# Kernel tuning notes

Hardware: AMD Instinct MI355X
Metric: run time of the kernel (lower is better)

## Reference

```python
import math
import jax, jax.numpy as jnp
import numpy as np

B, N, C = 2, 2048, 4096
NUM_HEADS, KV_HEADS, HEAD_DIM = 32, 8, 128
N_REP = NUM_HEADS // KV_HEADS  # num_key_value_groups
MAX_SEQ = 4096


def rotate_half(x):
    h = x.shape[-1] // 2
    return jnp.concatenate([-x[..., h:], x[..., :h]], axis=-1)


def setup_inputs() -> dict:
    key = jax.random.key(0)
    k1, k2 = jax.random.split(key)
    inp = jax.random.normal(k1, (B, N, C), jnp.float32)
    sz = NUM_HEADS * HEAD_DIM + 2 * KV_HEADS * HEAD_DIM  # 6144
    weight = jax.random.normal(k2, (sz, C), jnp.float32) * 0.02
    # real LLaMA rotary caches [1,1,MAX_SEQ,HEAD_DIM]
    inv_freq = 1.0 / (10000.0 ** (jnp.arange(0, HEAD_DIM, 2, dtype=jnp.float32) / HEAD_DIM))
    t = jnp.arange(MAX_SEQ, dtype=jnp.float32)
    freqs = jnp.outer(t, inv_freq)
    emb = jnp.concatenate([freqs, freqs], axis=-1)
    cos_cached = jnp.cos(emb)[None, None]
    sin_cached = jnp.sin(emb)[None, None]
    neg = jnp.finfo(jnp.float32).min
    causal = jnp.where(jnp.tril(jnp.ones((N, N), dtype=bool)), 0.0, neg)
    attention_mask = jnp.broadcast_to(causal[None, None], (B, 1, N, N))
    position_ids = jnp.broadcast_to(jnp.arange(N, dtype=jnp.int32), (B, N))
    observation_mask = jnp.ones((B, N), dtype=jnp.int32)
    return dict(input=inp, weight=weight, cos_cached=cos_cached, sin_cached=sin_cached,
                attention_mask=attention_mask, position_ids=position_ids,
                observation_mask=observation_mask)


def reference(input, weight, cos_cached, sin_cached, attention_mask, position_ids, observation_mask):
    b, n, c = input.shape
    dtype = input.dtype
    qkv = input @ weight.T  # [B,N,6144]
    sz_q = NUM_HEADS * HEAD_DIM
    sz_kv = KV_HEADS * HEAD_DIM
    q = qkv[:, :, :sz_q].reshape(b, n, NUM_HEADS, HEAD_DIM).transpose(0, 2, 1, 3)
    k = qkv[:, :, sz_q:sz_q + sz_kv].reshape(b, n, KV_HEADS, HEAD_DIM).transpose(0, 2, 1, 3)
    v = qkv[:, :, sz_q + sz_kv:].reshape(b, n, KV_HEADS, HEAD_DIM).transpose(0, 2, 1, 3)
    # inline RoPE (HF llama apply_rotary_pos_emb)
    cos = cos_cached[0, 0][position_ids][:, None]  # [B,1,N,D]
    sin = sin_cached[0, 0][position_ids][:, None]
    q = q * cos + rotate_half(q) * sin
    k = k * cos + rotate_half(k) * sin
    # repeat_kv: expand kv heads to match q heads (each kv head repeated contiguously)
    k = jnp.repeat(k, N_REP, axis=1)
    v = jnp.repeat(v, N_REP, axis=1)
    attn = jnp.einsum('bhqd,bhkd->bhqk', q / math.sqrt(HEAD_DIM), k)
    attn = attn + attention_mask
    attn = jnp.maximum(attn, jnp.finfo(dtype).min)
    attn = jax.nn.softmax(attn.astype(jnp.float32), axis=-1).astype(dtype)
    out = jnp.einsum('bhqk,bhkd->bqhd', attn, v).reshape(b, n, c)
    # output[observation_mask == 1]: with an all-ones mask this is the flat [B*N, C] output;
    # expressed jit-safely as a multiplicative select
    out = out.reshape(b * n, c) * (observation_mask.reshape(-1, 1) == 1)
    return out.astype(jnp.float32)
```

## Files before the change

kernel.cpp:

```cpp
#include <hip/hip_runtime.h>
#include <hip/hip_bf16.h>
#include <stdint.h>

typedef __attribute__((ext_vector_type(8))) short bf16x8;
typedef __attribute__((ext_vector_type(4))) float f32x4;
typedef __attribute__((ext_vector_type(16))) float f32x16;

#define NB 2
#define NSEQ 2048
#define CDIM 4096
#define NH 32
#define NKV 8
#define HD 128
#define QKV_COLS 6144

static __device__ __forceinline__ unsigned short f2bf(float f) {
    union { float f; unsigned int u; } v; v.f = f;
    unsigned int r = v.u + 0x7fff + ((v.u >> 16) & 1);
    return (unsigned short)(r >> 16);
}
static __device__ __forceinline__ float bf2f(unsigned short b) {
    union { unsigned int u; float f; } v; v.u = ((unsigned int)b) << 16;
    return v.f;
}

static __device__ __forceinline__ void glds16(const void* g, void* l) {
    __builtin_amdgcn_global_load_lds(
        (const __attribute__((address_space(1))) void*)g,
        (__attribute__((address_space(3))) void*)l, 16, 0, 0);
}

static __device__ __forceinline__ unsigned cvtpk(float a, float b) {
    unsigned r; asm("v_cvt_pk_bf16_f32 %0, %1, %2" : "=v"(r) : "v"(a), "v"(b));
    return r;
}

static __device__ __forceinline__ void pack_tile(const f32x16& p, int l, bf16x8& fa, bf16x8& fb) {
    unsigned a0 = cvtpk(p[0], p[1]),   b0 = cvtpk(p[4], p[5]);
    unsigned a1 = cvtpk(p[2], p[3]),   b1 = cvtpk(p[6], p[7]);
    unsigned a2 = cvtpk(p[8], p[9]),   b2 = cvtpk(p[12], p[13]);
    unsigned a3 = cvtpk(p[10], p[11]), b3 = cvtpk(p[14], p[15]);
    union U { unsigned u[4]; bf16x8 v; } ua, ub;
#if __has_builtin(__builtin_amdgcn_permlane32_swap)
    auto r0 = __builtin_amdgcn_permlane32_swap(a0, b0, false, false);
    auto r1 = __builtin_amdgcn_permlane32_swap(a1, b1, false, false);
    auto r2 = __builtin_amdgcn_permlane32_swap(a2, b2, false, false);
    auto r3 = __builtin_amdgcn_permlane32_swap(a3, b3, false, false);
    ua.u[0] = r0[0]; ua.u[1] = r1[0]; ua.u[2] = r0[1]; ua.u[3] = r1[1];
    ub.u[0] = r2[0]; ub.u[1] = r3[0]; ub.u[2] = r2[1]; ub.u[3] = r3[1];
#else
    unsigned a0t = __shfl_xor(a0, 32), b0t = __shfl_xor(b0, 32);
    unsigned a1t = __shfl_xor(a1, 32), b1t = __shfl_xor(b1, 32);
    unsigned a2t = __shfl_xor(a2, 32), b2t = __shfl_xor(b2, 32);
    unsigned a3t = __shfl_xor(a3, 32), b3t = __shfl_xor(b3, 32);
    bool lo = (l < 32);
    ua.u[0] = lo ? a0 : b0t; ua.u[1] = lo ? a1 : b1t; ua.u[2] = lo ? a0t : b0; ua.u[3] = lo ? a1t : b1;
    ub.u[0] = lo ? a2 : b2t; ub.u[1] = lo ? a3 : b3t; ub.u[2] = lo ? a2t : b2; ub.u[3] = lo ? a3t : b3;
#endif
    fa = ua.v; fb = ub.v;
}

__global__ void convert_kernel(const float* __restrict__ inA, const float* __restrict__ inW,
                               unsigned short* __restrict__ outA, unsigned short* __restrict__ outW) {
    const long long nA4 = (long long)CDIM * (NB * NSEQ) / 4;
    const long long nW4 = (long long)QKV_COLS * CDIM / 4;
    const long long total = nA4 + nW4;
    for (long long i = blockIdx.x * 256LL + threadIdx.x; i < total; i += (long long)gridDim.x * 256LL) {
        const float4* src; unsigned short* dst; long long j;
        if (i < nA4) { src = (const float4*)inA; dst = outA; j = i; }
        else         { src = (const float4*)inW; dst = outW; j = i - nA4; }
        float4 v = src[j];
        ushort4 o;
        o.x = f2bf(v.x); o.y = f2bf(v.y); o.z = f2bf(v.z); o.w = f2bf(v.w);
        ((ushort4*)dst)[j] = o;
    }
}

#define GEMM_PHASE(PP, VNSTR, LOADB) do {                                                     \
    const int r0_ = wm*128 + (PP*2)*16 + lr16;                                                \
    bf16x8 a00 = *(const bf16x8*)(lds + cur*32768 + r0_*128 + ((lc4*16) ^ ((r0_&7)<<4)));     \
    bf16x8 a01 = *(const bf16x8*)(lds + cur*32768 + r0_*128 + ((64+lc4*16) ^ ((r0_&7)<<4)));  \
    const int r1_ = r0_ + 16;                                                                 \
    bf16x8 a10 = *(const bf16x8*)(lds + cur*32768 + r1_*128 + ((lc4*16) ^ ((r1_&7)<<4)));     \
    bf16x8 a11 = *(const bf16x8*)(lds + cur*32768 + r1_*128 + ((64+lc4*16) ^ ((r1_&7)<<4)));  \
    if (LOADB) {                                                                              \
        _Pragma("unroll")                                                                     \
        for (int ni = 0; ni < 4; ++ni) {                                                      \
            int rb = wn*64 + ni*16 + lr16;                                                    \
            bfr[ni][0] = *(const bf16x8*)(lds + 65536 + cur*32768 + rb*128 + ((lc4*16) ^ ((rb&7)<<4)));    \
            bfr[ni][1] = *(const bf16x8*)(lds + 65536 + cur*32768 + rb*128 + ((64+lc4*16) ^ ((rb&7)<<4))); \
        }                                                                                     \
    }                                                                                         \
    if (PP == 0)      { stageB(tb, ktn, tid*16);         stageB(tb, ktn, 8192 + tid*16);  }   \
    else if (PP == 1) { stageB(tb, ktn, 16384 + tid*16); stageB(tb, ktn, 24576 + tid*16); }   \
    else if (PP == 2) { stageA(tb, ktn, abase);          stageA(tb, ktn, abase + 4096);   }   \
    else              { stageA(tb, ktn, abase + 8192);   stageA(tb, ktn, abase + 12288);  }   \
    __builtin_amdgcn_s_barrier();                                                             \
    asm volatile("s_waitcnt lgkmcnt(0)" ::: "memory");                                        \
    __builtin_amdgcn_s_setprio(1);                                                            \
    _Pragma("unroll")                                                                         \
    for (int ni = 0; ni < 4; ++ni) {                                                          \
        acc[PP*2  ][ni] = __builtin_amdgcn_mfma_f32_16x16x32_bf16(a00, bfr[ni][0], acc[PP*2  ][ni], 0,0,0); \
        acc[PP*2  ][ni] = __builtin_amdgcn_mfma_f32_16x16x32_bf16(a01, bfr[ni][1], acc[PP*2  ][ni], 0,0,0); \
        acc[PP*2+1][ni] = __builtin_amdgcn_mfma_f32_16x16x32_bf16(a10, bfr[ni][0], acc[PP*2+1][ni], 0,0,0); \
        acc[PP*2+1][ni] = __builtin_amdgcn_mfma_f32_16x16x32_bf16(a11, bfr[ni][1], acc[PP*2+1][ni], 0,0,0); \
    }                                                                                         \
    __builtin_amdgcn_s_setprio(0);                                                            \
    asm volatile("s_waitcnt " VNSTR ::: "memory");                                            \
    __builtin_amdgcn_s_barrier();                                                             \
} while (0)

__global__ __launch_bounds__(512) void gemm_qkv8(
    const unsigned short* __restrict__ A, const unsigned short* __restrict__ W,
    unsigned short* __restrict__ qb, unsigned short* __restrict__ kb, unsigned short* __restrict__ vt)
{
    __shared__ unsigned char lds[131072];
    const int bid0 = blockIdx.x;
    const int swz = (bid0 & 7) * 48 + (bid0 >> 3);
    const int bm = swz & 15, bn = swz >> 4;
    const int tid = threadIdx.x, l = tid & 63, w = tid >> 6;
    const int wm = w >> 2, wn = w & 3;
    const int lr16 = l & 15, lc4 = l >> 4;
    const int abase = (tid >> 8) * 16384 + (tid & 255) * 16;

    f32x4 acc[8][4] = {};
    bf16x8 bfr[4][2];

    auto stageB = [&](int tb, int ktn, int d) {
        int r = d >> 7, c = d & 127;
        int cs = c ^ ((r & 7) << 4);
        glds16(W + (long long)(bn * 256 + r) * CDIM + ktn * 64 + (cs >> 1),
               lds + 65536 + tb * 32768 + d);
    };
    auto stageA = [&](int tb, int ktn, int d) {
        int r = d >> 7, c = d & 127;
        int cs = c ^ ((r & 7) << 4);
        glds16(A + (long long)(bm * 256 + r) * CDIM + ktn * 64 + (cs >> 1),
               lds + tb * 32768 + d);
    };

    stageB(0, 0, tid * 16);         stageB(0, 0, 8192 + tid * 16);
    stageB(0, 0, 16384 + tid * 16); stageB(0, 0, 24576 + tid * 16);
    stageA(0, 0, abase);            stageA(0, 0, abase + 4096);
    stageA(0, 0, abase + 8192);     stageA(0, 0, abase + 12288);
    asm volatile("s_waitcnt vmcnt(0)" ::: "memory");
    __builtin_amdgcn_s_barrier();

    for (int t = 0; t < 64; ++t) {
        const int cur = t & 1, tb = cur ^ 1;
        const int ktn = (t + 1 < 64) ? t + 1 : 63;
        GEMM_PHASE(0, "vmcnt(4)", 1);
        GEMM_PHASE(1, "vmcnt(5)", 0);
        GEMM_PHASE(2, "vmcnt(6)", 0);
        GEMM_PHASE(3, "vmcnt(3)", 0);
    }

    const int colq = bn * 256 + wn * 64;
#pragma unroll
    for (int mf = 0; mf < 8; ++mf) {
        int gm0 = bm * 256 + wm * 128 + mf * 16 + lc4 * 4;
        int b = gm0 >> 11, n0 = gm0 & 2047;
#pragma unroll
        for (int nf = 0; nf < 4; ++nf) {
            int coln = colq + nf * 16 + lr16;
            if (bn < 16) {
                unsigned short* dst = qb + (((long long)(b * NH + (coln >> 7)) * NSEQ + n0) << 7) + (coln & 127);
#pragma unroll
                for (int r = 0; r < 4; ++r) dst[(long long)r << 7] = f2bf(acc[mf][nf][r]);
            } else if (bn < 20) {
                int ck = coln - 4096;
                unsigned short* dst = kb + (((long long)(b * NKV + (ck >> 7)) * NSEQ + n0) << 7) + (ck & 127);
#pragma unroll
                for (int r = 0; r < 4; ++r) dst[(long long)r << 7] = f2bf(acc[mf][nf][r]);
            } else {
                int cv = coln - 5120;
                ushort4 o4;
                o4.x = f2bf(acc[mf][nf][0]); o4.y = f2bf(acc[mf][nf][1]);
                o4.z = f2bf(acc[mf][nf][2]); o4.w = f2bf(acc[mf][nf][3]);
                *(ushort4*)(vt + (((long long)(b * NKV + (cv >> 7)) * HD + (cv & 127)) << 11) + n0) = o4;
            }
        }
    }
}

__global__ void rope_kernel(unsigned short* __restrict__ qb, unsigned short* __restrict__ kb,
                            const float* __restrict__ cosc, const float* __restrict__ sinc,
                            const int* __restrict__ pos) {
    int rowid = blockIdx.x * 4 + (threadIdx.x >> 6);
    int d = threadIdx.x & 63;
    int b = rowid / (40 * NSEQ);
    int rem = rowid % (40 * NSEQ);
    int head = rem / NSEQ, n = rem % NSEQ;
    unsigned short* p;
    float scale;
    if (head < NH) { p = qb + (((long long)(b * NH + head) * NSEQ + n) << 7); scale = 0.12751747934e0f; }
    else           { p = kb + (((long long)(b * NKV + (head - NH)) * NSEQ + n) << 7); scale = 1.0f; }
    int pid = pos[b * NSEQ + n];
    float c = cosc[pid * HD + d], s = sinc[pid * HD + d];
    float x0 = bf2f(p[d]), x1 = bf2f(p[d + 64]);
    p[d]      = f2bf((x0 * c - x1 * s) * scale);
    p[d + 64] = f2bf((x1 * c + x0 * s) * scale);
}

__global__ __launch_bounds__(256) void attn_kernel(
    const unsigned short* __restrict__ qb, const unsigned short* __restrict__ kb,
    const unsigned short* __restrict__ vt, const int* __restrict__ obs,
    float* __restrict__ out)
{
    __shared__ unsigned char k_tile[16384];
    __shared__ unsigned char v_tile[16384];

    const int bid = blockIdx.x;
    const int qt = 15 - (bid >> 6);
    const int bh = bid & 63;
    const int b = bh >> 5, h = bh & 31, kvh = h >> 2;
    const int t = threadIdx.x, l = t & 63, w = t >> 6;
    const int lr = l & 31, hi = l >> 5;
    const int swl = (l & 7) << 4;

    const unsigned short* Qb = qb + (((long long)(b * NH + h) * NSEQ + qt * 128 + w * 32) << 7);
    const unsigned short* Kb = kb + (((long long)(b * NKV + kvh) * NSEQ) << 7);
    const unsigned short* Vb = vt + (((long long)(b * NKV + kvh) * HD) << 11);

    bf16x8 qf[8];
#pragma unroll
    for (int dk = 0; dk < 8; ++dk)
        qf[dk] = *(const bf16x8*)(Qb + lr * 128 + dk * 16 + hi * 8);

    f32x16 o[4];
#pragma unroll
    for (int dt = 0; dt < 4; ++dt)
#pragma unroll
        for (int e = 0; e < 16; ++e) o[dt][e] = 0.f;
    float m_run = -1e30f, l_run = 0.f;

    const int qwmax = qt * 128 + w * 32 + 31;
    const int niter = 2 * qt + 2;

    for (int kt = 0; kt < niter; ++kt) {
#pragma unroll
        for (int i = 0; i < 4; ++i) {
            int byte = (i * 256 + t) * 16;
            { int r = byte >> 8, c = byte & 255; int cs = c ^ ((r & 7) << 4);
              glds16(Kb + (((long long)(kt * 64 + r)) << 7) + (cs >> 1), k_tile + byte); }
            { int r = byte >> 7, c = byte & 127; int cs = c ^ ((r & 7) << 4);
              glds16(Vb + (((long long)r) << 11) + kt * 64 + (cs >> 1), v_tile + byte); }
        }
        __syncthreads();

        if (kt * 64 <= qwmax) {
            f32x16 s0, s1;
#pragma unroll
            for (int e = 0; e < 16; ++e) { s0[e] = 0.f; s1[e] = 0.f; }
            __builtin_amdgcn_s_setprio(1);
#pragma unroll
            for (int dk = 0; dk < 8; ++dk) {
                int cb = (dk * 32 + hi * 16) ^ swl;
                bf16x8 k0 = *(const bf16x8*)(k_tile + lr * 256 + cb);
                bf16x8 k1 = *(const bf16x8*)(k_tile + (32 + lr) * 256 + cb);
                s0 = __builtin_amdgcn_mfma_f32_32x32x16_bf16(k0, qf[dk], s0, 0, 0, 0);
                s1 = __builtin_amdgcn_mfma_f32_32x32x16_bf16(k1, qf[dk], s1, 0, 0, 0);
            }
            __builtin_amdgcn_s_setprio(0);

            if (kt * 64 + 63 > qt * 128 + w * 32) {
                int qg = qt * 128 + w * 32 + lr;
                int base = kt * 64 + hi * 4;
#pragma unroll
                for (int e = 0; e < 16; ++e) {
                    int kv0 = base + (e & 3) + 8 * (e >> 2);
                    if (kv0 > qg)      s0[e] = -1e30f;
                    if (kv0 + 32 > qg) s1[e] = -1e30f;
                }
            }

            float mloc = fmaxf(s0[0], s0[1]);
#pragma unroll
            for (int e = 2; e < 16; ++e) mloc = fmaxf(mloc, s0[e]);
#pragma unroll
            for (int e = 0; e < 16; ++e) mloc = fmaxf(mloc, s1[e]);
            mloc = fmaxf(mloc, __shfl_xor(mloc, 32));

            float mm = m_run;
            if (!__all(mloc - m_run <= 8.f)) {
                mm = fmaxf(m_run, mloc);
                float sc = __builtin_amdgcn_exp2f(m_run - mm);
                l_run *= sc;
#pragma unroll
                for (int dt = 0; dt < 4; ++dt)
#pragma unroll
                    for (int e = 0; e < 16; ++e) o[dt][e] *= sc;
                m_run = mm;
            }
            float sum = 0.f;
#pragma unroll
            for (int e = 0; e < 16; ++e) { s0[e] = __builtin_amdgcn_exp2f(s0[e] - mm); sum += s0[e]; }
#pragma unroll
            for (int e = 0; e < 16; ++e) { s1[e] = __builtin_amdgcn_exp2f(s1[e] - mm); sum += s1[e]; }
            sum += __shfl_xor(sum, 32);
            l_run += sum;

            bf16x8 pb[4];
            pack_tile(s0, l, pb[0], pb[1]);
            pack_tile(s1, l, pb[2], pb[3]);

            __builtin_amdgcn_s_setprio(1);
#pragma unroll
            for (int dt = 0; dt < 4; ++dt) {
#pragma unroll
                for (int kk = 0; kk < 4; ++kk) {
                    int cb = (kk * 32 + hi * 16) ^ swl;
                    bf16x8 vf = *(const bf16x8*)(v_tile + (dt * 32 + lr) * 128 + cb);
                    o[dt] = __builtin_amdgcn_mfma_f32_32x32x16_bf16(vf, pb[kk], o[dt], 0, 0, 0);
                }
            }
            __builtin_amdgcn_s_setprio(0);
        }
        __syncthreads();
    }

    {
        int n = qt * 128 + w * 32 + lr;
        float fac = (1.f / l_run) * ((obs[b * NSEQ + n] == 1) ? 1.f : 0.f);
        unsigned char* slice = k_tile + w * 4096;
        int q2 = l >> 1, half = l & 1;
        long long orow = ((long long)(b * NSEQ + qt * 128 + w * 32 + q2)) << 12;
#pragma unroll
        for (int dt = 0; dt < 4; ++dt) {
#pragma unroll
            for (int e = 0; e < 16; e += 2) {
                int dl = (e & 3) + 8 * (e >> 2) + hi * 4;
                int byte = (lr * 128 + dl * 4) ^ ((lr & 7) << 4);
                *(float2*)(slice + byte) = make_float2(o[dt][e] * fac, o[dt][e + 1] * fac);
            }
#pragma unroll
            for (int j = 0; j < 4; ++j) {
                int byte = (q2 * 128 + half * 64 + j * 16) ^ ((q2 & 7) << 4);
                f32x4 vv = *(const f32x4*)(slice + byte);
                *(f32x4*)(out + orow + h * 128 + dt * 32 + half * 16 + j * 4) = vv;
            }
            __syncthreads();
        }
    }
}

extern "C" void kernel_launch(void* const* d_in, const int* in_sizes, int n_in,
                              void* d_out, int out_size, void* d_ws, size_t ws_size,
                              hipStream_t stream) {
    (void)in_sizes; (void)n_in; (void)out_size; (void)ws_size;
    const float* inp  = (const float*)d_in[0];
    const float* wgt  = (const float*)d_in[1];
    const float* cosc = (const float*)d_in[2];
    const float* sinc = (const float*)d_in[3];
    const int* pos = (const int*)d_in[5];
    const int* obs = (const int*)d_in[6];
    float* out = (float*)d_out;

    char* ws = (char*)d_ws;
    unsigned short* A16 = (unsigned short*)(ws);
    unsigned short* W16 = (unsigned short*)(ws + 33554432LL);
    unsigned short* qb  = (unsigned short*)(ws + 83886080LL);
    unsigned short* kb  = (unsigned short*)(ws + 117440512LL);
    unsigned short* vt  = (unsigned short*)(ws + 125829120LL);

    convert_kernel<<<2048, 256, 0, stream>>>(inp, wgt, A16, W16);
    gemm_qkv8<<<384, 512, 0, stream>>>(A16, W16, qb, kb, vt);
    rope_kernel<<<(2 * 40 * NSEQ) / 4, 256, 0, stream>>>(qb, kb, cosc, sinc, pos);
    attn_kernel<<<16 * 64, 256, 0, stream>>>(qb, kb, vt, obs, out);
}
```

Measured before the change: 417.3 us.

## Widen QKV GEMM tile to 256x384 with single-buffered LDS staging

The QKV projection GEMM now uses 256x384 output tiles: each wave computes 128x96, so 256 workgroups are launched instead of 384, which on a 256-CU part is a single wave of blocks. The double-buffered LDS is replaced by one 80KB buffer, and next-tile loads are interleaved across the four phases with new vmcnt waits. The epilogue now routes each column to Q, K or V by column index, since a tile can span regions. This raises register pressure (48 accumulators) and makes the single-buffer load ordering more fragile.

```diff
diff --git a/kernel.cpp b/kernel.cpp
--- a/kernel.cpp
+++ b/kernel.cpp
@@ -76,98 +76,92 @@
     }
 }
 
-#define GEMM_PHASE(PP, VNSTR, LOADB) do {                                                     \
+#define GPHASE(PP, VNSTR, STAGES) do {                                                        \
     const int r0_ = wm*128 + (PP*2)*16 + lr16;                                                \
-    bf16x8 a00 = *(const bf16x8*)(lds + cur*32768 + r0_*128 + ((lc4*16) ^ ((r0_&7)<<4)));     \
-    bf16x8 a01 = *(const bf16x8*)(lds + cur*32768 + r0_*128 + ((64+lc4*16) ^ ((r0_&7)<<4)));  \
     const int r1_ = r0_ + 16;                                                                 \
-    bf16x8 a10 = *(const bf16x8*)(lds + cur*32768 + r1_*128 + ((lc4*16) ^ ((r1_&7)<<4)));     \
-    bf16x8 a11 = *(const bf16x8*)(lds + cur*32768 + r1_*128 + ((64+lc4*16) ^ ((r1_&7)<<4)));  \
-    if (LOADB) {                                                                              \
+    bf16x8 a00 = *(const bf16x8*)(lds + r0_*128 + ((lc4*16) ^ ((r0_&7)<<4)));                 \
+    bf16x8 a01 = *(const bf16x8*)(lds + r0_*128 + ((64+lc4*16) ^ ((r0_&7)<<4)));              \
+    bf16x8 a10 = *(const bf16x8*)(lds + r1_*128 + ((lc4*16) ^ ((r1_&7)<<4)));                 \
+    bf16x8 a11 = *(const bf16x8*)(lds + r1_*128 + ((64+lc4*16) ^ ((r1_&7)<<4)));              \
+    if (PP == 0) {                                                                            \
         _Pragma("unroll")                                                                     \
-        for (int ni = 0; ni < 4; ++ni) {                                                      \
-            int rb = wn*64 + ni*16 + lr16;                                                    \
-            bfr[ni][0] = *(const bf16x8*)(lds + 65536 + cur*32768 + rb*128 + ((lc4*16) ^ ((rb&7)<<4)));    \
-            bfr[ni][1] = *(const bf16x8*)(lds + 65536 + cur*32768 + rb*128 + ((64+lc4*16) ^ ((rb&7)<<4))); \
+        for (int nf = 0; nf < 6; ++nf) {                                                      \
+            int rb = wn*96 + nf*16 + lr16;                                                    \
+            bfr[nf][0] = *(const bf16x8*)(lds + 32768 + rb*128 + ((lc4*16) ^ ((rb&7)<<4)));   \
+            bfr[nf][1] = *(const bf16x8*)(lds + 32768 + rb*128 + ((64+lc4*16) ^ ((rb&7)<<4)));\
         }                                                                                     \
     }                                                                                         \
-    if (PP == 0)      { stageB(tb, ktn, tid*16);         stageB(tb, ktn, 8192 + tid*16);  }   \
-    else if (PP == 1) { stageB(tb, ktn, 16384 + tid*16); stageB(tb, ktn, 24576 + tid*16); }   \
-    else if (PP == 2) { stageA(tb, ktn, abase);          stageA(tb, ktn, abase + 4096);   }   \
-    else              { stageA(tb, ktn, abase + 8192);   stageA(tb, ktn, abase + 12288);  }   \
+    STAGES;                                                                                   \
     __builtin_amdgcn_s_barrier();                                                             \
     asm volatile("s_waitcnt lgkmcnt(0)" ::: "memory");                                        \
     __builtin_amdgcn_s_setprio(1);                                                            \
     _Pragma("unroll")                                                                         \
-    for (int ni = 0; ni < 4; ++ni) {                                                          \
-        acc[PP*2  ][ni] = __builtin_amdgcn_mfma_f32_16x16x32_bf16(a00, bfr[ni][0], acc[PP*2  ][ni], 0,0,0); \
-        acc[PP*2  ][ni] = __builtin_amdgcn_mfma_f32_16x16x32_bf16(a01, bfr[ni][1], acc[PP*2  ][ni], 0,0,0); \
-        acc[PP*2+1][ni] = __builtin_amdgcn_mfma_f32_16x16x32_bf16(a10, bfr[ni][0], acc[PP*2+1][ni], 0,0,0); \
-        acc[PP*2+1][ni] = __builtin_amdgcn_mfma_f32_16x16x32_bf16(a11, bfr[ni][1], acc[PP*2+1][ni], 0,0,0); \
+    for (int nf = 0; nf < 6; ++nf) {                                                          \
+        acc[PP*2  ][nf] = __builtin_amdgcn_mfma_f32_16x16x32_bf16(a00, bfr[nf][0], acc[PP*2  ][nf], 0,0,0); \
+        acc[PP*2  ][nf] = __builtin_amdgcn_mfma_f32_16x16x32_bf16(a01, bfr[nf][1], acc[PP*2  ][nf], 0,0,0); \
+        acc[PP*2+1][nf] = __builtin_amdgcn_mfma_f32_16x16x32_bf16(a10, bfr[nf][0], acc[PP*2+1][nf], 0,0,0); \
+        acc[PP*2+1][nf] = __builtin_amdgcn_mfma_f32_16x16x32_bf16(a11, bfr[nf][1], acc[PP*2+1][nf], 0,0,0); \
     }                                                                                         \
     __builtin_amdgcn_s_setprio(0);                                                            \
     asm volatile("s_waitcnt " VNSTR ::: "memory");                                            \
     __builtin_amdgcn_s_barrier();                                                             \
 } while (0)
 
-__global__ __launch_bounds__(512) void gemm_qkv8(
+__global__ __launch_bounds__(512, 2) void gemm_qkv8(
     const unsigned short* __restrict__ A, const unsigned short* __restrict__ W,
     unsigned short* __restrict__ qb, unsigned short* __restrict__ kb, unsigned short* __restrict__ vt)
 {
-    __shared__ unsigned char lds[131072];
+    __shared__ unsigned char lds[81920];
     const int bid0 = blockIdx.x;
-    const int swz = (bid0 & 7) * 48 + (bid0 >> 3);
+    const int swz = (bid0 & 7) * 32 + (bid0 >> 3);
     const int bm = swz & 15, bn = swz >> 4;
     const int tid = threadIdx.x, l = tid & 63, w = tid >> 6;
     const int wm = w >> 2, wn = w & 3;
     const int lr16 = l & 15, lc4 = l >> 4;
     const int abase = (tid >> 8) * 16384 + (tid & 255) * 16;
 
-    f32x4 acc[8][4] = {};
-    bf16x8 bfr[4][2];
-
-    auto stageB = [&](int tb, int ktn, int d) {
+    f32x4 acc[8][6] = {};
+    bf16x8 bfr[6][2];
+
+    auto stageA = [&](int kt, int d) {
         int r = d >> 7, c = d & 127;
         int cs = c ^ ((r & 7) << 4);
-        glds16(W + (long long)(bn * 256 + r) * CDIM + ktn * 64 + (cs >> 1),
-               lds + 65536 + tb * 32768 + d);
+        glds16(A + (long long)(bm * 256 + r) * CDIM + kt * 64 + (cs >> 1), lds + d);
     };
-    auto stageA = [&](int tb, int ktn, int d) {
+    auto stageB = [&](int kt, int d) {
         int r = d >> 7, c = d & 127;
         int cs = c ^ ((r & 7) << 4);
-        glds16(A + (long long)(bm * 256 + r) * CDIM + ktn * 64 + (cs >> 1),
-               lds + tb * 32768 + d);
+        glds16(W + (long long)(bn * 384 + r) * CDIM + kt * 64 + (cs >> 1), lds + 32768 + d);
     };
 
-    stageB(0, 0, tid * 16);         stageB(0, 0, 8192 + tid * 16);
-    stageB(0, 0, 16384 + tid * 16); stageB(0, 0, 24576 + tid * 16);
-    stageA(0, 0, abase);            stageA(0, 0, abase + 4096);
-    stageA(0, 0, abase + 8192);     stageA(0, 0, abase + 12288);
+    stageB(0, tid * 16);           stageB(0, tid * 16 + 8192);
+    stageB(0, tid * 16 + 16384);   stageB(0, tid * 16 + 24576);
+    stageB(0, tid * 16 + 32768);   stageB(0, tid * 16 + 40960);
+    stageA(0, abase);              stageA(0, abase + 4096);
+    stageA(0, abase + 8192);
     asm volatile("s_waitcnt vmcnt(0)" ::: "memory");
     __builtin_amdgcn_s_barrier();
 
     for (int t = 0; t < 64; ++t) {
-        const int cur = t & 1, tb = cur ^ 1;
-        const int ktn = (t + 1 < 64) ? t + 1 : 63;
-        GEMM_PHASE(0, "vmcnt(4)", 1);
-        GEMM_PHASE(1, "vmcnt(5)", 0);
-        GEMM_PHASE(2, "vmcnt(6)", 0);
-        GEMM_PHASE(3, "vmcnt(3)", 0);
-    }
-
-    const int colq = bn * 256 + wn * 64;
+        const int tn = (t + 1 < 64) ? t + 1 : 63;
+        GPHASE(0, "vmcnt(2)", { stageA(t, abase + 12288); });
+        GPHASE(1, "vmcnt(4)", { stageB(tn, tid*16); stageB(tn, tid*16 + 8192); stageB(tn, tid*16 + 16384); });
+        GPHASE(2, "vmcnt(7)", { stageB(tn, tid*16 + 24576); stageB(tn, tid*16 + 32768); stageB(tn, tid*16 + 40960); stageA(tn, abase); });
+        GPHASE(3, "vmcnt(2)", { stageA(tn, abase + 4096); stageA(tn, abase + 8192); });
+    }
+
 #pragma unroll
     for (int mf = 0; mf < 8; ++mf) {
         int gm0 = bm * 256 + wm * 128 + mf * 16 + lc4 * 4;
         int b = gm0 >> 11, n0 = gm0 & 2047;
 #pragma unroll
-        for (int nf = 0; nf < 4; ++nf) {
-            int coln = colq + nf * 16 + lr16;
-            if (bn < 16) {
+        for (int nf = 0; nf < 6; ++nf) {
+            int coln = bn * 384 + wn * 96 + nf * 16 + lr16;
+            if (coln < 4096) {
                 unsigned short* dst = qb + (((long long)(b * NH + (coln >> 7)) * NSEQ + n0) << 7) + (coln & 127);
 #pragma unroll
                 for (int r = 0; r < 4; ++r) dst[(long long)r << 7] = f2bf(acc[mf][nf][r]);
-            } else if (bn < 20) {
+            } else if (coln < 5120) {
                 int ck = coln - 4096;
                 unsigned short* dst = kb + (((long long)(b * NKV + (ck >> 7)) * NSEQ + n0) << 7) + (ck & 127);
 #pragma unroll
@@ -364,7 +358,7 @@
     unsigned short* vt  = (unsigned short*)(ws + 125829120LL);
 
     convert_kernel<<<2048, 256, 0, stream>>>(inp, wgt, A16, W16);
-    gemm_qkv8<<<384, 512, 0, stream>>>(A16, W16, qb, kb, vt);
+    gemm_qkv8<<<256, 512, 0, stream>>>(A16, W16, qb, kb, vt);
     rope_kernel<<<(2 * 40 * NSEQ) / 4, 256, 0, stream>>>(qb, kb, cosc, sinc, pos);
     attn_kernel<<<16 * 64, 256, 0, stream>>>(qb, kb, vt, obs, out);
 }
```

Result: slower. 626.3 us (+50.1%).
